# Optimization experiments

Measured on AMD Instinct MI355X. Metric: run time of the kernel, lower is better.

The kernel has to match this reference:

```python
import jax, jax.numpy as jnp
import numpy as np

N_SAMPLES = 1024   # self.n
B = 128            # batch of x
DIM = 64           # latent dim (self.dim)
DX = 64            # observation dim
K = 16             # annealing steps
N_LEAP = 3         # leapfrog inner steps
STEP = 0.05        # leapfrog step size
LOGVAR_P = 0.0     # momentum log-variance
LOG2PI = float(np.log(2.0 * np.pi))


def _betas():
    # beta_unnorm = sigmoid(4*(2*linspace(0,1,K+2)-1)); normalized to [0,1]
    b = jax.nn.sigmoid(4.0 * (2.0 * jnp.linspace(0.0, 1.0, K + 2) - 1.0))
    return (b - b[0]) / (b[-1] - b[0])


def _logprob_normal(z, logvar=0.0):
    return -0.5 * (LOG2PI + logvar + z * z * jnp.exp(-logvar))


def setup_inputs() -> dict:
    key = jax.random.key(0)
    k1, k2, k3, k4, k5 = jax.random.split(key, 5)
    x = jax.random.normal(k1, (B, DX), jnp.float32)
    W_enc = jax.random.normal(k2, (DX, DIM), jnp.float32) / jnp.sqrt(float(DX))
    W_dec = jax.random.normal(k3, (DIM, DX), jnp.float32) / jnp.sqrt(float(DIM))
    q_noise = jax.random.normal(k4, (N_SAMPLES, B, DIM), jnp.float32)
    p_noise = jax.random.normal(k5, (N_SAMPLES, B, DIM), jnp.float32)
    return {"x": x, "W_enc": W_enc, "W_dec": W_dec, "q_noise": q_noise, "p_noise": p_noise}


def reference(x, W_enc, W_dec, q_noise, p_noise):
    beta = _betas()
    mu = x @ W_enc  # (B, DIM) importance mean

    def loglik(q):  # Gaussian decoder logN(x | q @ W_dec, I), shape (n, B)
        r = jnp.einsum('nbd,de->nbe', q, W_dec)
        return _logprob_normal(x - r).sum(-1)

    def prior_lp(q):
        return _logprob_normal(q).sum(-1)

    def imp_lp(q):
        return _logprob_normal(q - mu).sum(-1)

    def w(q):  # functional: loglik + log prior - log importance
        return loglik(q) + prior_lp(q) - imp_lp(q)

    # initial samples from importance distr, initial momentum
    q0 = mu + q_noise                       # (n, B, DIM)
    p0 = jnp.exp(0.5 * LOGVAR_P) * p_noise  # (n, B, DIM)
    slw0 = (beta[1] - beta[0]) * w(q0)      # incremental weight at k=0

    noise_key = jax.random.key(42)

    def step(carry, inp):
        q, p, slw = carry
        bk, bkp1, kidx = inp
        # momentum refresh: v = 0 => full resample
        p = jnp.exp(0.5 * LOGVAR_P) * jax.random.normal(
            jax.random.fold_in(noise_key, kidx), q.shape, q.dtype)

        def tgt(qq):  # annealed target at beta_k (scalar for grad)
            return (bk * (loglik(qq) + prior_lp(qq)) + (1.0 - bk) * imp_lp(qq)).sum()

        g = jax.grad(tgt)
        for _ in range(N_LEAP):  # standard leapfrog
            p = p + 0.5 * STEP * g(q)
            q = q + STEP * p * jnp.exp(-LOGVAR_P)
            p = p + 0.5 * STEP * g(q)
        # NOTE: original torch accept/reject assignment is a no-op (chained
        # advanced indexing writes into a copy), so z_new is always kept.
        slw = slw + (bkp1 - bk) * w(q)
        return (q, p, slw), None

    ks = jnp.arange(1, K + 1)
    (qf, pf, slw), _ = jax.lax.scan(step, (q0, p0, slw0), (beta[1:K + 1], beta[2:K + 2], ks))
    return jax.scipy.special.logsumexp(slw, axis=0) - jnp.log(float(N_SAMPLES))
```

## Files before the change

### kernel.cpp

```cpp
#include <hip/hip_runtime.h>
#include <math.h>
#include <stdint.h>


#define WS_A     0
#define WS_MU    4096
#define WS_C     12288
#define WS_XSQ   20480
#define WS_AMU   20608
#define WS_F     28800
#define WS_WC    36992
#define WS_V     37120
#define WS_LAM   41216
#define WS_FZ    41280
#define WS_VF    49472
#define WS_SLW   53568
#define WS_TOTAL (WS_SLW + 131072)
#define WS_RNG   (WS_SLW + 131072)
#define STEP_U32 8388608ull

#define LOG2PI 1.8378770664093453f

typedef _Float16 half8_t __attribute__((ext_vector_type(8)));
typedef float f4_t __attribute__((ext_vector_type(4)));
typedef unsigned int uint4_t __attribute__((ext_vector_type(4)));

struct KParams {
  float beta[18];
  float dbeta[17];
  uint32_t fk0[16];
  uint32_t fk1[16];
};

__host__ __device__ static inline void threefry2x32(uint32_t ks0, uint32_t ks1,
                                                    uint32_t x0, uint32_t x1,
                                                    uint32_t& o0, uint32_t& o1) {
  uint32_t ks2 = ks0 ^ ks1 ^ 0x1BD11BDAu;
  x0 += ks0; x1 += ks1;
#define TFR(r) { x0 += x1; x1 = (x1 << (r)) | (x1 >> (32 - (r))); x1 ^= x0; }
  TFR(13) TFR(15) TFR(26) TFR(6)
  x0 += ks1; x1 += ks2 + 1u;
  TFR(17) TFR(29) TFR(16) TFR(24)
  x0 += ks2; x1 += ks0 + 2u;
  TFR(13) TFR(15) TFR(26) TFR(6)
  x0 += ks0; x1 += ks1 + 3u;
  TFR(17) TFR(29) TFR(16) TFR(24)
  x0 += ks1; x1 += ks2 + 4u;
  TFR(13) TFR(15) TFR(26) TFR(6)
  x0 += ks2; x1 += ks0 + 5u;
#undef TFR
  o0 = x0; o1 = x1;
}

__device__ __forceinline__ float u_from_bits(uint32_t bits) {
  const float LO = __uint_as_float(0xBF7FFFFFu);
  float f = __uint_as_float((bits >> 9) | 0x3F800000u) - 1.0f;
  return fmaf(f, 2.0f, LO);
}

__device__ __forceinline__ float erfinv_f(float x) {
  float w = -__logf(fmaf(-x, x, 1.0f));
  float p;
  if (w < 5.0f) {
    w -= 2.5f;
    p = 2.81022636e-08f;
    p = fmaf(p, w, 3.43273939e-07f);
    p = fmaf(p, w, -3.5233877e-06f);
    p = fmaf(p, w, -4.39150654e-06f);
    p = fmaf(p, w, 0.00021858087f);
    p = fmaf(p, w, -0.00125372503f);
    p = fmaf(p, w, -0.00417768164f);
    p = fmaf(p, w, 0.246640727f);
    p = fmaf(p, w, 1.50140941f);
  } else {
    w = sqrtf(w) - 3.0f;
    p = -0.000200214257f;
    p = fmaf(p, w, 0.000100950558f);
    p = fmaf(p, w, 0.00134934322f);
    p = fmaf(p, w, -0.00367342844f);
    p = fmaf(p, w, 0.00573950773f);
    p = fmaf(p, w, -0.0076224613f);
    p = fmaf(p, w, 0.00943887047f);
    p = fmaf(p, w, 1.00167406f);
    p = fmaf(p, w, 2.83297682f);
  }
  return p * x;
}

__global__ void k_setup1(const float* __restrict__ x, const float* __restrict__ Wenc,
                         const float* __restrict__ Wdec, float* __restrict__ ws) {
  int t = blockIdx.x * 256 + threadIdx.x;
  if (t < 4096) {
    int i = t >> 6, j = t & 63;
    float s = 0;
    for (int e = 0; e < 64; ++e) s = fmaf(Wdec[i*64+e], Wdec[j*64+e], s);
    ws[WS_A + t] = s;
  } else if (t < 12288) {
    int u = t - 4096; int b = u >> 6, d = u & 63;
    float s = 0;
    for (int e = 0; e < 64; ++e) s = fmaf(x[b*64+e], Wenc[e*64+d], s);
    ws[WS_MU + u] = s;
  } else if (t < 20480) {
    int u = t - 12288; int b = u >> 6, d = u & 63;
    float s = 0;
    for (int e = 0; e < 64; ++e) s = fmaf(x[b*64+e], Wdec[d*64+e], s);
    ws[WS_C + u] = s;
  } else if (t < 20608) {
    int b = t - 20480;
    float s = 0;
    for (int e = 0; e < 64; ++e) s = fmaf(x[b*64+e], x[b*64+e], s);
    ws[WS_XSQ + b] = s;
  }
}

#define DRAW(PC, IDX)                                                        \
  { uint32_t o0, o1;                                                         \
    threefry2x32(k0, k1, 0u, base + (IDX), o0, o1);                          \
    PC = 1.41421356f * erfinv_f(u_from_bits(o0 ^ o1)); }

#define PACKD(DST, DD)                                                       \
  { _Float16 hh = (_Float16)(DD);                                            \
    _Float16 ll = (_Float16)((DD) - (float)hh);                              \
    DST = (uint32_t)__builtin_bit_cast(unsigned short, hh) |                 \
          ((uint32_t)__builtin_bit_cast(unsigned short, ll) << 16); }

#define EP 65
__global__ __launch_bounds__(1024) void k_fused(float* __restrict__ ws, KParams P,
                                                int nRng, int nS, int Lcut) {
  const int blk = blockIdx.x;
  const int tid = threadIdx.x;
  if (blk == 0) {
    __shared__ float Am[64 * EP];
    __shared__ float Vm[64 * EP];
    __shared__ float cs_c[32], cs_s[32];
    __shared__ int ppu[32], ppv[32];
    for (int i = tid; i < 4096; i += 1024) {
      int r = i >> 6, c = i & 63;
      Am[r*EP + c] = ws[WS_A + i];
      Vm[r*EP + c] = (r == c) ? 1.0f : 0.0f;
    }
    const int pA = tid & 31;
    int uA = (pA == 0) ? 0 : pA;
    int vA = (pA == 0) ? 63 : (63 - pA);
    const int pV0 = tid >> 6;
    int uV0 = (pV0 == 0) ? 0 : pV0;
    int vV0 = (pV0 == 0) ? 63 : (63 - pV0);
    const int pV1 = 16 + pV0;
    int uV1 = pV1;
    int vV1 = 63 - pV1;
    __syncthreads();
    for (int sweep = 0; sweep < 3; ++sweep) {
      for (int r = 0; r < 63; ++r) {
        if (tid < 32) {
          float app = Am[uA*(EP+1)], aqq = Am[vA*(EP+1)], apq = Am[uA*EP+vA];
          float c = 1.0f, s = 0.0f;
          if (fabsf(apq) > 1e-30f) {
            float tau = (aqq - app) / (2.0f * apq);
            float t = copysignf(1.0f / (fabsf(tau) + sqrtf(fmaf(tau, tau, 1.0f))), tau);
            c = 1.0f / sqrtf(fmaf(t, t, 1.0f));
            s = t * c;
          }
          ppu[tid] = uA; ppv[tid] = vA; cs_c[tid] = c; cs_s[tid] = s;
        }
        __syncthreads();
        {
          int i = tid >> 5;
          int ui = ppu[i], vi = ppv[i];
          const int uj = uA, vj = vA;
          float ci = cs_c[i], si = cs_s[i], cj = cs_c[pA], sj = cs_s[pA];
          float a = Am[ui*EP+uj], bb = Am[ui*EP+vj];
          float d = Am[vi*EP+uj], e  = Am[vi*EP+vj];
          float r0u = ci*a  - si*d;
          float r1u = fmaf(si, a,  ci*d);
          float r0v = ci*bb - si*e;
          float r1v = fmaf(si, bb, ci*e);
          Am[ui*EP+uj] = cj*r0u - sj*r0v;
          Am[ui*EP+vj] = fmaf(sj, r0u, cj*r0v);
          Am[vi*EP+uj] = cj*r1u - sj*r1v;
          Am[vi*EP+vj] = fmaf(sj, r1u, cj*r1v);
        }
        {
          const int k = tid & 63;
          {
            float c2 = cs_c[pV0], s2 = cs_s[pV0];
            float vu = Vm[k*EP+uV0], vv = Vm[k*EP+vV0];
            Vm[k*EP+uV0] = c2*vu - s2*vv;
            Vm[k*EP+vV0] = fmaf(s2, vu, c2*vv);
          }
          {
            float c2 = cs_c[pV1], s2 = cs_s[pV1];
            float vu = Vm[k*EP+uV1], vv = Vm[k*EP+vV1];
            Vm[k*EP+uV1] = c2*vu - s2*vv;
            Vm[k*EP+vV1] = fmaf(s2, vu, c2*vv);
          }
        }
        uA  = (uA  == 0) ? 0 : ((uA  == 63) ? 1 : uA  + 1);
        vA  = (vA  == 63) ? 1 : vA  + 1;
        uV0 = (uV0 == 0) ? 0 : ((uV0 == 63) ? 1 : uV0 + 1);
        vV0 = (vV0 == 63) ? 1 : vV0 + 1;
        uV1 = (uV1 == 63) ? 1 : uV1 + 1;
        vV1 = (vV1 == 63) ? 1 : vV1 + 1;
        __syncthreads();
      }
    }
    for (int i = tid; i < 4096; i += 1024) ws[WS_V + i] = Vm[(i >> 6)*EP + (i & 63)];
    if (tid < 64) ws[WS_LAM + tid] = Am[tid*(EP+1)];
  } else if (blk <= nRng) {
    const int L = (blk - 1) * 1024 + tid;
    const int bI = L >> 8, t256 = L & 255;
    const int wv = t256 >> 6, lane = t256 & 63;
    const int cw = lane & 15, g4 = lane >> 4;
    const int koff = g4 * 8;
    const int trajBase = bI * 64 + wv * 16;
    const uint32_t base = (uint32_t)(trajBase + cw) * 64u;
    uint32_t* wsu = (uint32_t*)ws;
    const int nSteps = nS + ((nS < 16 && L < Lcut) ? 1 : 0);
    for (int j = 1; j <= nSteps; ++j) {
      const uint32_t k0 = P.fk0[j-1], k1 = P.fk1[j-1];
      uint32_t ov[16];
#pragma unroll
      for (int i = 0; i < 8; ++i) { float dd; DRAW(dd, koff + i) PACKD(ov[i], dd) }
#pragma unroll
      for (int i = 0; i < 8; ++i) { float dd; DRAW(dd, 32 + koff + i) PACKD(ov[8+i], dd) }
      uint4_t* wr = (uint4_t*)(wsu + WS_RNG + (size_t)(j-1)*STEP_U32 + (size_t)L*16u);
      wr[0] = (uint4_t){ov[0], ov[1], ov[2], ov[3]};
      wr[1] = (uint4_t){ov[4], ov[5], ov[6], ov[7]};
      wr[2] = (uint4_t){ov[8], ov[9], ov[10], ov[11]};
      wr[3] = (uint4_t){ov[12], ov[13], ov[14], ov[15]};
    }
  } else {
    int t = (blk - 1 - nRng) * 1024 + tid;
    if (t < 8192) {
      int b = t >> 6, d = t & 63;
      float s = 0;
      for (int m = 0; m < 64; ++m) s = fmaf(ws[WS_MU + b*64+m], ws[WS_A + m*64+d], s);
      ws[WS_AMU + t] = s;
      ws[WS_F + t] = ws[WS_C + t] - ws[WS_MU + t] - s;
    }
  }
}

__global__ void k_setupfv(float* __restrict__ ws) {
  int blk = blockIdx.x;
  if (blk < 32) {
    int t = blk * 256 + threadIdx.x;
    int b = t >> 6, d = t & 63;
    float s = 0;
    for (int m = 0; m < 64; ++m) s = fmaf(ws[WS_F + b*64+m], ws[WS_V + m*64+d], s);
    ws[WS_FZ + t] = s;
  } else if (blk < 36) {
    int idx = (blk - 32) * 256 + threadIdx.x;
    int lane = idx & 63, F = idx >> 6;
    int t = F >> 3, kt = (F >> 2) & 1, nt = F & 3;
    int n = nt*16 + (lane & 15);
    int k0 = kt*32 + ((lane >> 4) & 3)*8;
    uint32_t out[4];
    for (int jj = 0; jj < 4; ++jj) {
      float v0 = ws[WS_V + (k0 + 2*jj    )*64 + n];
      float v1 = ws[WS_V + (k0 + 2*jj + 1)*64 + n];
      _Float16 h0, h1;
      if (t == 0) { h0 = (_Float16)v0; h1 = (_Float16)v1; }
      else {
        _Float16 a0 = (_Float16)v0, a1 = (_Float16)v1;
        h0 = (_Float16)(v0 - (float)a0);
        h1 = (_Float16)(v1 - (float)a1);
      }
      unsigned short u0 = __builtin_bit_cast(unsigned short, h0);
      unsigned short u1 = __builtin_bit_cast(unsigned short, h1);
      out[jj] = (uint32_t)u0 | ((uint32_t)u1 << 16);
    }
    uint32_t* dst = (uint32_t*)ws + WS_VF + idx*4;
    dst[0] = out[0]; dst[1] = out[1]; dst[2] = out[2]; dst[3] = out[3];
  } else {
    int b = threadIdx.x;
    if (b < 128) {
      float muc = 0, musq = 0, muamu = 0;
      for (int d = 0; d < 64; ++d) {
        float m = ws[WS_MU + b*64+d];
        muc   = fmaf(m, ws[WS_C + b*64+d], muc);
        musq  = fmaf(m, m, musq);
        muamu = fmaf(m, ws[WS_AMU + b*64+d], muamu);
      }
      ws[WS_WC + b] = -32.0f * LOG2PI - 0.5f * ws[WS_XSQ + b]
                      + muc - 0.5f * musq - 0.5f * muamu;
    }
  }
}


#define SPLIT1(AH, AL, J, VV)                                                \
  { _Float16 hh = (_Float16)(VV); AH[J] = hh;                                \
    AL[J] = (_Float16)((VV) - (float)hh); }

#define DRAWSPLIT8(AH, AL, KB)                                               \
  { float dd;                                                                \
    DRAW(dd, (KB)+0) SPLIT1(AH, AL, 0, dd)                                   \
    DRAW(dd, (KB)+1) SPLIT1(AH, AL, 1, dd)                                   \
    DRAW(dd, (KB)+2) SPLIT1(AH, AL, 2, dd)                                   \
    DRAW(dd, (KB)+3) SPLIT1(AH, AL, 3, dd)                                   \
    DRAW(dd, (KB)+4) SPLIT1(AH, AL, 4, dd)                                   \
    DRAW(dd, (KB)+5) SPLIT1(AH, AL, 5, dd)                                   \
    DRAW(dd, (KB)+6) SPLIT1(AH, AL, 6, dd)                                   \
    DRAW(dd, (KB)+7) SPLIT1(AH, AL, 7, dd) }

#define FRAGB(T, KT, NT)                                                     \
  __builtin_bit_cast(half8_t, VF[(((T)*2+(KT))*4+(NT))*64 + lane])

#define ROT1(ZO, NT, AH0, AL0, AH1, AL1)                                     \
  { half8_t bh0 = FRAGB(0,0,NT), bh1 = FRAGB(0,1,NT);                        \
    half8_t bl0 = FRAGB(1,0,NT), bl1 = FRAGB(1,1,NT);                        \
    f4_t aa = {0.f, 0.f, 0.f, 0.f};                                          \
    aa = __builtin_amdgcn_mfma_f32_16x16x32_f16(AH0, bh0, aa, 0, 0, 0);      \
    aa = __builtin_amdgcn_mfma_f32_16x16x32_f16(AH1, bh1, aa, 0, 0, 0);      \
    aa = __builtin_amdgcn_mfma_f32_16x16x32_f16(AL0, bh0, aa, 0, 0, 0);      \
    aa = __builtin_amdgcn_mfma_f32_16x16x32_f16(AL1, bh1, aa, 0, 0, 0);      \
    aa = __builtin_amdgcn_mfma_f32_16x16x32_f16(AH0, bl0, aa, 0, 0, 0);      \
    aa = __builtin_amdgcn_mfma_f32_16x16x32_f16(AH1, bl1, aa, 0, 0, 0);      \
    ZO = aa; }

#define ROTATE4(O0, O1, O2, O3, AH0, AL0, AH1, AL1)                          \
  ROT1(O0, 0, AH0, AL0, AH1, AL1) ROT1(O1, 1, AH0, AL0, AH1, AL1)            \
  ROT1(O2, 2, AH0, AL0, AH1, AL1) ROT1(O3, 3, AH0, AL0, AH1, AL1)

#define LF4V(ZV, PV, NLM, FV, DBL)                                           \
  { f4_t gg = __builtin_elementwise_fma(bk4,                                 \
        __builtin_elementwise_fma(NLM, ZV, FV), -ZV);                        \
    PV = __builtin_elementwise_fma(c025v, gg, PV);                           \
    if (DBL) PV = __builtin_elementwise_fma(c025v, gg, PV);                  \
    ZV = __builtin_elementwise_fma(c005v, PV, ZV); }
#define SUBSTEPV(DBL)                                                        \
  LF4V(z0, pz0, nlm0, fzv0, DBL) LF4V(z1, pz1, nlm1, fzv1, DBL)              \
  LF4V(z2, pz2, nlm2, fzv2, DBL) LF4V(z3, pz3, nlm3, fzv3, DBL)

#define W_EVALN(WOUT)                                                        \
  { f4_t s1 = fzv0*z0 + fzv1*z1 + fzv2*z2 + fzv3*z3;                         \
    f4_t s2 = (lmS0*z0)*z0 + (lmS1*z1)*z1 + (lmS2*z2)*z2 + (lmS3*z3)*z3;     \
    f4_t vv = s1 - 0.5f*s2;                                                  \
    float r0 = vv.x, r1 = vv.y, r2 = vv.z, r3 = vv.w;                        \
    r0 += __shfl_xor(r0, 1); r1 += __shfl_xor(r1, 1);                        \
    r2 += __shfl_xor(r2, 1); r3 += __shfl_xor(r3, 1);                        \
    r0 += __shfl_xor(r0, 2); r1 += __shfl_xor(r1, 2);                        \
    r2 += __shfl_xor(r2, 2); r3 += __shfl_xor(r3, 2);                        \
    r0 += __shfl_xor(r0, 4); r1 += __shfl_xor(r1, 4);                        \
    r2 += __shfl_xor(r2, 4); r3 += __shfl_xor(r3, 4);                        \
    r0 += __shfl_xor(r0, 8); r1 += __shfl_xor(r1, 8);                        \
    r2 += __shfl_xor(r2, 8); r3 += __shfl_xor(r3, 8);                        \
    float wsel = (cw == 0) ? r0 : ((cw == 1) ? r1 : ((cw == 2) ? r2 : r3));  \
    WOUT = wsel + wcs; }

#define PLO 0x05040100u
#define PHI 0x07060302u

__global__ __launch_bounds__(256) void k_main(const float* __restrict__ qn,
                                              const float* __restrict__ ws,
                                              float* __restrict__ slw_out,
                                              KParams P, int nS, int Lcut) {
  __shared__ uint4_t VF[1024];
  const int tid = threadIdx.x;
  {
    const uint4_t* src = (const uint4_t*)((const uint32_t*)ws + WS_VF);
    for (int i = tid; i < 1024; i += 256) VF[i] = src[i];
  }
  __syncthreads();

  const int lane = tid & 63;
  const int wv = tid >> 6;
  const int cw = lane & 15;
  const int g4 = lane >> 4;
  const int koff = g4 * 8;
  const int trajBase = blockIdx.x * 64 + wv * 16;
  const uint32_t base = (uint32_t)(trajBase + cw) * 64u;
  const int Lme = blockIdx.x * 256 + tid;

  const int b0 = (trajBase + g4*4 + 0) & 127;
  const int b1 = (trajBase + g4*4 + 1) & 127;
  const int b2 = (trajBase + g4*4 + 2) & 127;
  const int b3 = (trajBase + g4*4 + 3) & 127;
  f4_t fzv0, fzv1, fzv2, fzv3;
  fzv0.x = ws[WS_FZ + b0*64 + cw];      fzv0.y = ws[WS_FZ + b1*64 + cw];
  fzv0.z = ws[WS_FZ + b2*64 + cw];      fzv0.w = ws[WS_FZ + b3*64 + cw];
  fzv1.x = ws[WS_FZ + b0*64 + 16 + cw]; fzv1.y = ws[WS_FZ + b1*64 + 16 + cw];
  fzv1.z = ws[WS_FZ + b2*64 + 16 + cw]; fzv1.w = ws[WS_FZ + b3*64 + 16 + cw];
  fzv2.x = ws[WS_FZ + b0*64 + 32 + cw]; fzv2.y = ws[WS_FZ + b1*64 + 32 + cw];
  fzv2.z = ws[WS_FZ + b2*64 + 32 + cw]; fzv2.w = ws[WS_FZ + b3*64 + 32 + cw];
  fzv3.x = ws[WS_FZ + b0*64 + 48 + cw]; fzv3.y = ws[WS_FZ + b1*64 + 48 + cw];
  fzv3.z = ws[WS_FZ + b2*64 + 48 + cw]; fzv3.w = ws[WS_FZ + b3*64 + 48 + cw];
  const float lmS0 = ws[WS_LAM + cw];
  const float lmS1 = ws[WS_LAM + 16 + cw];
  const float lmS2 = ws[WS_LAM + 32 + cw];
  const float lmS3 = ws[WS_LAM + 48 + cw];
  const float wcs = ws[WS_WC + ((trajBase + g4*4 + (cw & 3)) & 127)];
  const f4_t nlm0 = {-lmS0, -lmS0, -lmS0, -lmS0};
  const f4_t nlm1 = {-lmS1, -lmS1, -lmS1, -lmS1};
  const f4_t nlm2 = {-lmS2, -lmS2, -lmS2, -lmS2};
  const f4_t nlm3 = {-lmS3, -lmS3, -lmS3, -lmS3};
  const f4_t c025v = {0.025f, 0.025f, 0.025f, 0.025f};
  const f4_t c005v = {0.05f, 0.05f, 0.05f, 0.05f};

  f4_t z0, z1, z2, z3, pz0, pz1, pz2, pz3;
  float slw = 0.0f;

  {
    const float* qp = qn + (size_t)base;
    f4_t qa = *(const f4_t*)(qp + koff);
    f4_t qb = *(const f4_t*)(qp + koff + 4);
    f4_t qc = *(const f4_t*)(qp + 32 + koff);
    f4_t qd = *(const f4_t*)(qp + 32 + koff + 4);
    half8_t ah0, al0, ah1, al1;
    SPLIT1(ah0, al0, 0, qa.x) SPLIT1(ah0, al0, 1, qa.y)
    SPLIT1(ah0, al0, 2, qa.z) SPLIT1(ah0, al0, 3, qa.w)
    SPLIT1(ah0, al0, 4, qb.x) SPLIT1(ah0, al0, 5, qb.y)
    SPLIT1(ah0, al0, 6, qb.z) SPLIT1(ah0, al0, 7, qb.w)
    SPLIT1(ah1, al1, 0, qc.x) SPLIT1(ah1, al1, 1, qc.y)
    SPLIT1(ah1, al1, 2, qc.z) SPLIT1(ah1, al1, 3, qc.w)
    SPLIT1(ah1, al1, 4, qd.x) SPLIT1(ah1, al1, 5, qd.y)
    SPLIT1(ah1, al1, 6, qd.z) SPLIT1(ah1, al1, 7, qd.w)
    ROTATE4(z0, z1, z2, z3, ah0, al0, ah1, al1)
  }
  {
    float w0;
    W_EVALN(w0);
    slw = fmaf(P.dbeta[0], w0, slw);
  }

  for (int j = 1; j <= 16; ++j) {
    const float bk = P.beta[j];
    const f4_t bk4 = {bk, bk, bk, bk};
    half8_t ah0, al0, ah1, al1;
    if (j <= nS || (j == nS + 1 && Lme < Lcut)) {
      const uint32_t* rp = (const uint32_t*)ws + WS_RNG
                         + (size_t)(j-1)*STEP_U32 + (size_t)Lme*16u;
      const uint4_t* rr = (const uint4_t*)rp;
      uint4_t q0 = rr[0], q1 = rr[1], q2 = rr[2], q3 = rr[3];
      uint4_t uh0 = { __builtin_amdgcn_perm(q0.y, q0.x, PLO),
                      __builtin_amdgcn_perm(q0.w, q0.z, PLO),
                      __builtin_amdgcn_perm(q1.y, q1.x, PLO),
                      __builtin_amdgcn_perm(q1.w, q1.z, PLO) };
      uint4_t ul0 = { __builtin_amdgcn_perm(q0.y, q0.x, PHI),
                      __builtin_amdgcn_perm(q0.w, q0.z, PHI),
                      __builtin_amdgcn_perm(q1.y, q1.x, PHI),
                      __builtin_amdgcn_perm(q1.w, q1.z, PHI) };
      uint4_t uh1 = { __builtin_amdgcn_perm(q2.y, q2.x, PLO),
                      __builtin_amdgcn_perm(q2.w, q2.z, PLO),
                      __builtin_amdgcn_perm(q3.y, q3.x, PLO),
                      __builtin_amdgcn_perm(q3.w, q3.z, PLO) };
      uint4_t ul1 = { __builtin_amdgcn_perm(q2.y, q2.x, PHI),
                      __builtin_amdgcn_perm(q2.w, q2.z, PHI),
                      __builtin_amdgcn_perm(q3.y, q3.x, PHI),
                      __builtin_amdgcn_perm(q3.w, q3.z, PHI) };
      ah0 = __builtin_bit_cast(half8_t, uh0);
      al0 = __builtin_bit_cast(half8_t, ul0);
      ah1 = __builtin_bit_cast(half8_t, uh1);
      al1 = __builtin_bit_cast(half8_t, ul1);
    } else {
      const uint32_t k0 = P.fk0[j-1], k1 = P.fk1[j-1];
      DRAWSPLIT8(ah0, al0, koff)
      DRAWSPLIT8(ah1, al1, 32 + koff)
    }
    ROTATE4(pz0, pz1, pz2, pz3, ah0, al0, ah1, al1)
    SUBSTEPV(false)
    SUBSTEPV(true)
    SUBSTEPV(true)
    float wj;
    W_EVALN(wj);
    slw = fmaf(P.dbeta[j], wj, slw);
  }
  if (cw < 4) slw_out[trajBase + g4*4 + cw] = slw;
}

__global__ void k_reduce(const float* __restrict__ slw, float* __restrict__ out) {
  __shared__ float red[256];
  int b = blockIdx.x, t = threadIdx.x;
  float v0 = slw[t*128 + b];
  float v1 = slw[(t+256)*128 + b];
  float v2 = slw[(t+512)*128 + b];
  float v3 = slw[(t+768)*128 + b];
  float m = fmaxf(fmaxf(v0, v1), fmaxf(v2, v3));
  red[t] = m; __syncthreads();
  for (int s = 128; s > 0; s >>= 1) {
    if (t < s) red[t] = fmaxf(red[t], red[t+s]);
    __syncthreads();
  }
  m = red[0]; __syncthreads();
  float sum = expf(v0 - m) + expf(v1 - m) + expf(v2 - m) + expf(v3 - m);
  red[t] = sum; __syncthreads();
  for (int s = 128; s > 0; s >>= 1) {
    if (t < s) red[t] += red[t+s];
    __syncthreads();
  }
  if (t == 0) out[b] = m + logf(red[0]) - 6.93147180559945309f;
}

extern "C" void kernel_launch(void* const* d_in, const int* in_sizes, int n_in,
                              void* d_out, int out_size, void* d_ws, size_t ws_size,
                              hipStream_t stream) {
  const float* x    = (const float*)d_in[0];
  const float* Wenc = (const float*)d_in[1];
  const float* Wdec = (const float*)d_in[2];
  const float* qn   = (const float*)d_in[3];
  float* ws  = (float*)d_ws;
  float* out = (float*)d_out;
  if (ws_size < (size_t)WS_TOTAL * sizeof(float)) return;

  size_t avail_u32 = ws_size / 4;
  int nS = 0, Lcut = 0;
  if (avail_u32 > (size_t)WS_RNG) {
    size_t r = avail_u32 - (size_t)WS_RNG;
    nS = (int)(r / STEP_U32);
    if (nS > 16) nS = 16;
    if (nS < 16) {
      size_t rem = r - (size_t)nS * STEP_U32;
      size_t lc = (rem / 16) & ~(size_t)63;
      if (lc > 524288) lc = 524288;
      Lcut = (int)lc;
    }
  }
  const int nRng = (nS > 0 || Lcut > 0) ? 512 : 0;

  KParams P;
  double bb[18];
  for (int i = 0; i < 18; ++i) {
    double tt = (double)i / 17.0;
    bb[i] = 1.0 / (1.0 + exp(-(8.0 * tt - 4.0)));
  }
  for (int i = 0; i < 18; ++i) P.beta[i] = (float)((bb[i] - bb[0]) / (bb[17] - bb[0]));
  for (int j = 0; j <= 16; ++j) P.dbeta[j] = P.beta[j+1] - P.beta[j];
  for (int k = 1; k <= 16; ++k) {
    uint32_t a, c;
    threefry2x32(0u, 42u, 0u, (uint32_t)k, a, c);
    P.fk0[k-1] = a; P.fk1[k-1] = c;
  }

  hipLaunchKernelGGL(k_setup1, dim3(81), dim3(256), 0, stream, x, Wenc, Wdec, ws);
  hipLaunchKernelGGL(k_fused, dim3(1 + nRng + 8), dim3(1024), 0, stream, ws, P, nRng, nS, Lcut);
  hipLaunchKernelGGL(k_setupfv, dim3(37), dim3(256), 0, stream, ws);
  hipLaunchKernelGGL(k_main, dim3(2048), dim3(256), 0, stream, qn, ws, ws + WS_SLW, P, nS, Lcut);
  hipLaunchKernelGGL(k_reduce, dim3(128), dim3(256), 0, stream, ws + WS_SLW, out);
}
```

Measured before the change: 572.8 us.

## Fold setupfv work into fused kernel block 0 using a global atomic flag

```diff
diff --git a/kernel.cpp b/kernel.cpp
--- a/kernel.cpp
+++ b/kernel.cpp
@@ -15,8 +15,9 @@
 #define WS_FZ    41280
 #define WS_VF    49472
 #define WS_SLW   53568
-#define WS_TOTAL (WS_SLW + 131072)
-#define WS_RNG   (WS_SLW + 131072)
+#define WS_FLG   (WS_SLW + 131072)
+#define WS_RNG   (WS_FLG + 64)
+#define WS_TOTAL WS_RNG
 #define STEP_U32 8388608ull
 
 #define LOG2PI 1.8378770664093453f
@@ -110,6 +111,8 @@
     float s = 0;
     for (int e = 0; e < 64; ++e) s = fmaf(x[b*64+e], x[b*64+e], s);
     ws[WS_XSQ + b] = s;
+  } else if (t == 20700) {
+    ((int*)ws)[WS_FLG] = 0;
   }
 }
 
@@ -203,8 +206,54 @@
         __syncthreads();
       }
     }
-    for (int i = tid; i < 4096; i += 1024) ws[WS_V + i] = Vm[(i >> 6)*EP + (i & 63)];
     if (tid < 64) ws[WS_LAM + tid] = Am[tid*(EP+1)];
+    if (tid == 0) {
+      while (atomicAdd((int*)ws + WS_FLG, 0) < 8) { }
+    }
+    __syncthreads();
+    __threadfence();
+    for (int t2 = tid; t2 < 8192; t2 += 1024) {
+      int b = t2 >> 6, d = t2 & 63;
+      float s = 0;
+      for (int m = 0; m < 64; ++m) s = fmaf(ws[WS_F + b*64+m], Vm[m*EP+d], s);
+      ws[WS_FZ + t2] = s;
+    }
+    {
+      int idx = tid;
+      int lane = idx & 63, Fr = idx >> 6;
+      int t = Fr >> 3, kt = (Fr >> 2) & 1, nt = Fr & 3;
+      int n = nt*16 + (lane & 15);
+      int k0 = kt*32 + ((lane >> 4) & 3)*8;
+      uint32_t out[4];
+      for (int jj = 0; jj < 4; ++jj) {
+        float v0 = Vm[(k0 + 2*jj    )*EP + n];
+        float v1 = Vm[(k0 + 2*jj + 1)*EP + n];
+        _Float16 h0, h1;
+        if (t == 0) { h0 = (_Float16)v0; h1 = (_Float16)v1; }
+        else {
+          _Float16 a0 = (_Float16)v0, a1 = (_Float16)v1;
+          h0 = (_Float16)(v0 - (float)a0);
+          h1 = (_Float16)(v1 - (float)a1);
+        }
+        unsigned short u0 = __builtin_bit_cast(unsigned short, h0);
+        unsigned short u1 = __builtin_bit_cast(unsigned short, h1);
+        out[jj] = (uint32_t)u0 | ((uint32_t)u1 << 16);
+      }
+      uint32_t* dst = (uint32_t*)ws + WS_VF + idx*4;
+      dst[0] = out[0]; dst[1] = out[1]; dst[2] = out[2]; dst[3] = out[3];
+    }
+    if (tid < 128) {
+      int b = tid;
+      float muc = 0, musq = 0, muamu = 0;
+      for (int d = 0; d < 64; ++d) {
+        float m = ws[WS_MU + b*64+d];
+        muc   = fmaf(m, ws[WS_C + b*64+d], muc);
+        musq  = fmaf(m, m, musq);
+        muamu = fmaf(m, ws[WS_AMU + b*64+d], muamu);
+      }
+      ws[WS_WC + b] = -32.0f * LOG2PI - 0.5f * ws[WS_XSQ + b]
+                      + muc - 0.5f * musq - 0.5f * muamu;
+    }
   } else if (blk <= nRng) {
     const int L = (blk - 1) * 1024 + tid;
     const int bI = L >> 8, t256 = L & 255;
@@ -237,52 +286,10 @@
       ws[WS_AMU + t] = s;
       ws[WS_F + t] = ws[WS_C + t] - ws[WS_MU + t] - s;
     }
-  }
-}
-
-__global__ void k_setupfv(float* __restrict__ ws) {
-  int blk = blockIdx.x;
-  if (blk < 32) {
-    int t = blk * 256 + threadIdx.x;
-    int b = t >> 6, d = t & 63;
-    float s = 0;
-    for (int m = 0; m < 64; ++m) s = fmaf(ws[WS_F + b*64+m], ws[WS_V + m*64+d], s);
-    ws[WS_FZ + t] = s;
-  } else if (blk < 36) {
-    int idx = (blk - 32) * 256 + threadIdx.x;
-    int lane = idx & 63, F = idx >> 6;
-    int t = F >> 3, kt = (F >> 2) & 1, nt = F & 3;
-    int n = nt*16 + (lane & 15);
-    int k0 = kt*32 + ((lane >> 4) & 3)*8;
-    uint32_t out[4];
-    for (int jj = 0; jj < 4; ++jj) {
-      float v0 = ws[WS_V + (k0 + 2*jj    )*64 + n];
-      float v1 = ws[WS_V + (k0 + 2*jj + 1)*64 + n];
-      _Float16 h0, h1;
-      if (t == 0) { h0 = (_Float16)v0; h1 = (_Float16)v1; }
-      else {
-        _Float16 a0 = (_Float16)v0, a1 = (_Float16)v1;
-        h0 = (_Float16)(v0 - (float)a0);
-        h1 = (_Float16)(v1 - (float)a1);
-      }
-      unsigned short u0 = __builtin_bit_cast(unsigned short, h0);
-      unsigned short u1 = __builtin_bit_cast(unsigned short, h1);
-      out[jj] = (uint32_t)u0 | ((uint32_t)u1 << 16);
-    }
-    uint32_t* dst = (uint32_t*)ws + WS_VF + idx*4;
-    dst[0] = out[0]; dst[1] = out[1]; dst[2] = out[2]; dst[3] = out[3];
-  } else {
-    int b = threadIdx.x;
-    if (b < 128) {
-      float muc = 0, musq = 0, muamu = 0;
-      for (int d = 0; d < 64; ++d) {
-        float m = ws[WS_MU + b*64+d];
-        muc   = fmaf(m, ws[WS_C + b*64+d], muc);
-        musq  = fmaf(m, m, musq);
-        muamu = fmaf(m, ws[WS_AMU + b*64+d], muamu);
-      }
-      ws[WS_WC + b] = -32.0f * LOG2PI - 0.5f * ws[WS_XSQ + b]
-                      + muc - 0.5f * musq - 0.5f * muamu;
+    __syncthreads();
+    if (tid == 0) {
+      __threadfence();
+      atomicAdd((int*)ws + WS_FLG, 1);
     }
   }
 }
@@ -533,7 +540,6 @@
 
   hipLaunchKernelGGL(k_setup1, dim3(81), dim3(256), 0, stream, x, Wenc, Wdec, ws);
   hipLaunchKernelGGL(k_fused, dim3(1 + nRng + 8), dim3(1024), 0, stream, ws, P, nRng, nS, Lcut);
-  hipLaunchKernelGGL(k_setupfv, dim3(37), dim3(256), 0, stream, ws);
   hipLaunchKernelGGL(k_main, dim3(2048), dim3(256), 0, stream, qn, ws, ws + WS_SLW, P, nS, Lcut);
   hipLaunchKernelGGL(k_reduce, dim3(128), dim3(256), 0, stream, ws + WS_SLW, out);
 }
```

Measured after the change: 583.8 us. About the same (+1.9%).
